# Performance work log

Measured on AMD Instinct MI355X. Metric: run time of the kernel, lower is better.

The kernel has to match this reference:

```python
import jax, jax.numpy as jnp
import numpy as np

TEMPERATURE = 0.04
LAMBDA_KOLEO = 0.1
EPS_NORM = 1e-12
EPS_KOLEO = 1e-9


def setup_inputs() -> dict:
    key = jax.random.key(0)
    k1, k2 = jax.random.split(key)
    N, D = 8192, 512
    z1 = jax.random.normal(k1, (N, D), dtype=jnp.float32)
    z2 = jax.random.normal(k2, (N, D), dtype=jnp.float32)
    return {"z1": z1, "z2": z2}


def _l2_normalize(x):
    # matches F.normalize(x, dim=1) with default eps=1e-12
    n = jnp.linalg.norm(x, axis=1, keepdims=True)
    return x / jnp.maximum(n, EPS_NORM)


def _infonce(queries, keys, temperature):
    # [N, N] similarity logits; labels are the diagonal
    logits = (queries @ keys.T) / temperature
    logp = jax.nn.log_softmax(logits, axis=1)
    return -jnp.mean(jnp.diagonal(logp))


def _koleo(emb):
    # pairwise euclidean distances via gram trick (matches torch.cdist p=2)
    sq = jnp.sum(emb * emb, axis=1)
    d2 = sq[:, None] + sq[None, :] - 2.0 * (emb @ emb.T)
    d = jnp.sqrt(jnp.maximum(d2, 0.0))
    N = emb.shape[0]
    eye = jnp.eye(N, dtype=bool)
    d = jnp.where(eye, jnp.inf, d)
    min_d = jnp.min(d, axis=1)
    return -jnp.mean(jnp.log(min_d + EPS_KOLEO))


def reference(z1, z2):
    z1 = _l2_normalize(z1)
    z2 = _l2_normalize(z2)
    loss_12 = _infonce(z1, z2, TEMPERATURE)
    loss_21 = _infonce(z2, z1, TEMPERATURE)
    loss_contrastive = (loss_12 + loss_21) / 2
    koleo_1 = _koleo(z1)
    koleo_2 = _koleo(z2)
    loss_koleo = (koleo_1 + koleo_2) / 2
    total_loss = loss_contrastive + LAMBDA_KOLEO * loss_koleo
    return total_loss
```

## Files before the change

### kernel.cpp

```cpp
#include <hip/hip_runtime.h>
#include <hip/hip_bf16.h>
#include <math.h>

#define N 8192
#define D 512
#define BM 128
#define BKB 128
#define NSTRIP 64
#define S_BLOCKS (NSTRIP * NSTRIP)
#define TRI (NSTRIP * (NSTRIP + 1) / 2)
#define G_BLOCKS (2 * TRI)
#define SG_BLOCKS (S_BLOCKS + G_BLOCKS)

typedef int i32x4 __attribute__((ext_vector_type(4)));

__device__ inline void gload_lds16(const void* g, void* l) {
  __builtin_amdgcn_global_load_lds(
      (const __attribute__((address_space(1))) void*)g,
      (__attribute__((address_space(3))) void*)l, 16, 0, 0);
}

__global__ __launch_bounds__(256) void norm_kernel(
    const float* __restrict__ z1, const float* __restrict__ z2,
    unsigned char* __restrict__ q1, unsigned char* __restrict__ q2,
    float* __restrict__ invs1, float* __restrict__ invs2,
    float* __restrict__ diag, float* __restrict__ out) {
  int row = blockIdx.x;
  int t = threadIdx.x;
  if (row == 0 && t == 0) out[0] = 0.0f;
  const float* a = z1 + (size_t)row * D;
  const float* b = z2 + (size_t)row * D;
  float va[2], vb[2];
  float ss1 = 0.f, ss2 = 0.f, dd = 0.f;
#pragma unroll
  for (int i = 0; i < 2; i++) {
    float x = a[t + 256 * i];
    float y = b[t + 256 * i];
    va[i] = x; vb[i] = y;
    ss1 += x * x; ss2 += y * y; dd += x * y;
  }
#pragma unroll
  for (int off = 1; off < 64; off <<= 1) {
    ss1 += __shfl_xor(ss1, off);
    ss2 += __shfl_xor(ss2, off);
    dd  += __shfl_xor(dd,  off);
  }
  __shared__ float red[3][4];
  int wv = t >> 6;
  if ((t & 63) == 0) { red[0][wv] = ss1; red[1][wv] = ss2; red[2][wv] = dd; }
  __syncthreads();
  ss1 = red[0][0] + red[0][1] + red[0][2] + red[0][3];
  ss2 = red[1][0] + red[1][1] + red[1][2] + red[1][3];
  dd  = red[2][0] + red[2][1] + red[2][2] + red[2][3];
  float i1 = 1.0f / fmaxf(sqrtf(ss1), 1e-12f);
  float i2 = 1.0f / fmaxf(sqrtf(ss2), 1e-12f);
  float m1 = 1e-30f, m2 = 1e-30f;
#pragma unroll
  for (int i = 0; i < 2; i++) {
    m1 = fmaxf(m1, fabsf(va[i] * i1));
    m2 = fmaxf(m2, fabsf(vb[i] * i2));
  }
#pragma unroll
  for (int off = 1; off < 64; off <<= 1) {
    m1 = fmaxf(m1, __shfl_xor(m1, off));
    m2 = fmaxf(m2, __shfl_xor(m2, off));
  }
  __syncthreads();
  if ((t & 63) == 0) { red[0][wv] = m1; red[1][wv] = m2; }
  __syncthreads();
  m1 = fmaxf(fmaxf(red[0][0], red[0][1]), fmaxf(red[0][2], red[0][3]));
  m2 = fmaxf(fmaxf(red[1][0], red[1][1]), fmaxf(red[1][2], red[1][3]));
  float s1 = 127.0f / m1, s2 = 127.0f / m2;
#pragma unroll
  for (int i = 0; i < 2; i++) {
    int qa = __float2int_rn(va[i] * i1 * s1);
    int qb = __float2int_rn(vb[i] * i2 * s2);
    q1[(size_t)row * D + t + 256 * i] = (unsigned char)qa;
    q2[(size_t)row * D + t + 256 * i] = (unsigned char)qb;
  }
  if (t == 0) {
    diag[row] = dd * i1 * i2;
    invs1[row] = m1 * (1.0f / 127.0f);
    invs2[row] = m2 * (1.0f / 127.0f);
  }
}

__device__ __forceinline__ void mm_tile_i8(
    const unsigned char* __restrict__ X, const unsigned char* __restrict__ Y,
    int r0, int c0, unsigned char* At, unsigned char* Bt, i32x4 (&acc)[4][4],
    int t, int lr, int quad, int rw, int cw) {
  const i32x4 izero = {0, 0, 0, 0};
#pragma unroll
  for (int i = 0; i < 4; i++)
#pragma unroll
    for (int j = 0; j < 4; j++) acc[i][j] = izero;

  for (int kc = 0; kc < 4; kc++) {
    int k0 = kc * BKB;
    __syncthreads();
#pragma unroll
    for (int it = 0; it < 4; it++) {
      int s = it * 256 + t;
      int row = s >> 3, cs = s & 7;
      int src = cs ^ (row & 7);
      gload_lds16(X + (size_t)(r0 + row) * D + k0 + src * 16, &At[s * 16]);
    }
#pragma unroll
    for (int it = 0; it < 4; it++) {
      int s = it * 256 + t;
      int row = s >> 3, cs = s & 7;
      int src = cs ^ (row & 7);
      gload_lds16(Y + (size_t)(c0 + row) * D + k0 + src * 16, &Bt[s * 16]);
    }
    __syncthreads();

#pragma unroll
    for (int step = 0; step < 2; step++) {
      i32x4 af[4], bf[4];
#pragma unroll
      for (int i = 0; i < 4; i++) {
        int row = rw * 64 + i * 16 + lr;
        int ps = (step * 4 + quad) ^ (row & 7);
        af[i] = *(const i32x4*)&At[row * BKB + ps * 16];
      }
#pragma unroll
      for (int j = 0; j < 4; j++) {
        int row = cw * 64 + j * 16 + lr;
        int ps = (step * 4 + quad) ^ (row & 7);
        bf[j] = *(const i32x4*)&Bt[row * BKB + ps * 16];
      }
#pragma unroll
      for (int i = 0; i < 4; i++)
#pragma unroll
        for (int j = 0; j < 4; j++)
          acc[i][j] = __builtin_amdgcn_mfma_i32_16x16x64_i8(af[i], bf[j], acc[i][j], 0, 0, 0);
    }
  }
}

__global__ __launch_bounds__(256, 3) void sg_kernel(
    const unsigned char* __restrict__ q1, const unsigned char* __restrict__ q2,
    const float* __restrict__ invs1, const float* __restrict__ invs2,
    float* __restrict__ rowS, float* __restrict__ colS,
    float* __restrict__ partG) {
  __shared__ unsigned char At[BM * BKB];
  __shared__ unsigned char Bt[BM * BKB];
  __shared__ float redA[2][BM];
  __shared__ float redB[2][BM];

  int bx = blockIdx.x;
  int t = threadIdx.x;
  int lane = t & 63;
  int wave = t >> 6;
  int quad = lane >> 4;
  int lr = lane & 15;
  int rw = wave >> 1;
  int cw = wave & 1;
  const float scalefac = 1.4426950408889634f / 0.04f;

  bool smode = bx < S_BLOCKS;
  const unsigned char* X;
  const unsigned char* Y;
  const float* ivA;
  const float* ivB;
  int r0, c0, ga = 0, gb = 0, gg = 0;
  bool diagb = false;
  if (smode) {
    r0 = (bx >> 6) * BM;
    c0 = (bx & 63) * BM;
    X = q1; Y = q2; ivA = invs1; ivB = invs2;
  } else {
    int gx = bx - S_BLOCKS;
    gg = (gx >= TRI) ? 1 : 0;
    int tri = gx - gg * TRI;
    int a = (int)((sqrtf(8.0f * (float)tri + 1.0f) - 1.0f) * 0.5f);
    while ((a + 1) * (a + 2) / 2 <= tri) a++;
    while (a * (a + 1) / 2 > tri) a--;
    int b = tri - a * (a + 1) / 2;
    ga = a; gb = b;
    X = gg ? q2 : q1; Y = X;
    ivA = gg ? invs2 : invs1; ivB = ivA;
    r0 = a * BM;
    c0 = b * BM;
    diagb = (a == b);
  }

  i32x4 acc[4][4];
  mm_tile_i8(X, Y, r0, c0, At, Bt, acc, t, lr, quad, rw, cw);

  float ia[4][4];
  float ib[4];
#pragma unroll
  for (int i = 0; i < 4; i++)
#pragma unroll
    for (int r = 0; r < 4; r++)
      ia[i][r] = ivA[r0 + rw * 64 + i * 16 + quad * 4 + r];
#pragma unroll
  for (int j = 0; j < 4; j++)
    ib[j] = ivB[c0 + cw * 64 + j * 16 + lr];

  if (smode) {
    float rowacc[4][4];
    float colacc[4] = {0.0f, 0.0f, 0.0f, 0.0f};
#pragma unroll
    for (int i = 0; i < 4; i++)
#pragma unroll
      for (int r = 0; r < 4; r++) rowacc[i][r] = 0.0f;
#pragma unroll
    for (int j = 0; j < 4; j++) ib[j] *= scalefac;
#pragma unroll
    for (int i = 0; i < 4; i++)
#pragma unroll
      for (int j = 0; j < 4; j++)
#pragma unroll
        for (int r = 0; r < 4; r++) {
          float e = __builtin_amdgcn_exp2f((float)acc[i][j][r] * ia[i][r] * ib[j]);
          rowacc[i][r] += e;
          colacc[j] += e;
        }
#pragma unroll
    for (int j = 0; j < 4; j++) {
      colacc[j] += __shfl_xor(colacc[j], 16);
      colacc[j] += __shfl_xor(colacc[j], 32);
    }
    if (lane < 16) {
#pragma unroll
      for (int j = 0; j < 4; j++) redA[rw][cw * 64 + j * 16 + lr] = colacc[j];
    }
    __syncthreads();
    if (t < BM) colS[(size_t)(r0 >> 7) * N + c0 + t] = redA[0][t] + redA[1][t];

#pragma unroll
    for (int i = 0; i < 4; i++)
#pragma unroll
      for (int r = 0; r < 4; r++) {
        float v = rowacc[i][r];
#pragma unroll
        for (int off = 1; off < 16; off <<= 1) v += __shfl_xor(v, off);
        if (lr == 0) redB[cw][rw * 64 + i * 16 + quad * 4 + r] = v;
      }
    __syncthreads();
    if (t < BM) rowS[(size_t)(c0 >> 7) * N + r0 + t] = redB[0][t] + redB[1][t];
  } else {
#pragma unroll
    for (int i = 0; i < 4; i++)
#pragma unroll
      for (int r = 0; r < 4; r++) {
        int rr = rw * 64 + i * 16 + quad * 4 + r;
        float v = -3.0e38f;
#pragma unroll
        for (int j = 0; j < 4; j++) {
          float x = (float)acc[i][j][r] * ib[j];
          int cc = cw * 64 + j * 16 + lr;
          if (diagb && cc == rr) x = -3.0e38f;
          v = fmaxf(v, x);
        }
#pragma unroll
        for (int off = 1; off < 16; off <<= 1) v = fmaxf(v, __shfl_xor(v, off));
        if (lr == 0) redA[cw][rr] = v * ia[i][r];
      }
    __syncthreads();
    if (t < BM)
      partG[((size_t)(gg * NSTRIP + gb)) * N + r0 + t] = fmaxf(redA[0][t], redA[1][t]);

    if (!diagb) {
#pragma unroll
      for (int j = 0; j < 4; j++) {
        float m = -3.0e38f;
#pragma unroll
        for (int i = 0; i < 4; i++)
#pragma unroll
          for (int r = 0; r < 4; r++) m = fmaxf(m, (float)acc[i][j][r] * ia[i][r]);
        m = fmaxf(m, __shfl_xor(m, 16));
        m = fmaxf(m, __shfl_xor(m, 32));
        if (lane < 16) redB[rw][cw * 64 + j * 16 + lr] = m * ib[j];
      }
      __syncthreads();
      if (t < BM)
        partG[((size_t)(gg * NSTRIP + ga)) * N + c0 + t] = fmaxf(redB[0][t], redB[1][t]);
    }
  }
}

__global__ __launch_bounds__(256) void combine_kernel(
    const float* __restrict__ diag,
    const float* __restrict__ rowS, const float* __restrict__ colS,
    const float* __restrict__ partG, float* __restrict__ out) {
  const float invT = 25.0f;
  int i = blockIdx.x * 256 + threadIdx.x;

  float s = 0.0f;
  for (int q = 0; q < NSTRIP; q++) s += rowS[(size_t)q * N + i];
  float a12 = logf(s) - diag[i] * invT;

  s = 0.0f;
  for (int o = 0; o < NSTRIP; o++) s += colS[(size_t)o * N + i];
  float a21 = logf(s) - diag[i] * invT;

  float g1 = -3.0e38f, g2 = -3.0e38f;
  for (int o = 0; o < NSTRIP; o++) {
    g1 = fmaxf(g1, partG[(size_t)o * N + i]);
    g2 = fmaxf(g2, partG[(size_t)(NSTRIP + o) * N + i]);
  }
  float k1 = logf(sqrtf(fmaxf(2.0f - 2.0f * g1, 0.0f)) + 1e-9f);
  float k2 = logf(sqrtf(fmaxf(2.0f - 2.0f * g2, 0.0f)) + 1e-9f);

  float c = 0.5f * (a12 + a21) / (float)N - 0.1f * 0.5f * (k1 + k2) / (float)N;
#pragma unroll
  for (int off = 1; off < 64; off <<= 1) c += __shfl_xor(c, off);
  __shared__ float fr[4];
  int wv = threadIdx.x >> 6;
  if ((threadIdx.x & 63) == 0) fr[wv] = c;
  __syncthreads();
  if (threadIdx.x == 0)
    atomicAdd(out, fr[0] + fr[1] + fr[2] + fr[3]);
}

extern "C" void kernel_launch(void* const* d_in, const int* in_sizes, int n_in,
                              void* d_out, int out_size, void* d_ws, size_t ws_size,
                              hipStream_t stream) {
  const float* z1 = (const float*)d_in[0];
  const float* z2 = (const float*)d_in[1];
  char* w = (char*)d_ws;
  unsigned char* q1 = (unsigned char*)w; w += (size_t)N * D;
  unsigned char* q2 = (unsigned char*)w; w += (size_t)N * D;
  float* invs1 = (float*)w;  w += (size_t)N * sizeof(float);
  float* invs2 = (float*)w;  w += (size_t)N * sizeof(float);
  float* diag = (float*)w;   w += (size_t)N * sizeof(float);
  float* rowS = (float*)w;   w += (size_t)NSTRIP * N * sizeof(float);
  float* colS = (float*)w;   w += (size_t)NSTRIP * N * sizeof(float);
  float* partG = (float*)w;  w += (size_t)2 * NSTRIP * N * sizeof(float);
  float* out = (float*)d_out;

  norm_kernel<<<N, 256, 0, stream>>>(z1, z2, q1, q2, invs1, invs2, diag, out);
  sg_kernel<<<SG_BLOCKS, 256, 0, stream>>>(q1, q2, invs1, invs2, rowS, colS, partG);
  combine_kernel<<<N / 256, 256, 0, stream>>>(diag, rowS, colS, partG, out);
}
```

Baseline: 202.2 us.

## Double-buffer int8 GEMM LDS tiles so global loads overlap MFMA compute

Splits the K loop into eight 64-byte chunks and alternates between two LDS buffer pairs. The loads for the next chunk are issued before the MFMAs on the current chunk, so global-to-LDS traffic can overlap compute instead of being followed by a full stall. The swizzle is adapted to 64-byte rows, and extra barriers are added before the epilogue reductions. Total LDS use stays the same. The gain depends on the barrier waiting for the async LDS loads correctly, and there are twice as many loop iterations, each with its own barrier.

```diff
diff --git a/kernel.cpp b/kernel.cpp
--- a/kernel.cpp
+++ b/kernel.cpp
@@ -5,7 +5,7 @@
 #define N 8192
 #define D 512
 #define BM 128
-#define BKB 128
+#define BK 64
 #define NSTRIP 64
 #define S_BLOCKS (NSTRIP * NSTRIP)
 #define TRI (NSTRIP * (NSTRIP + 1) / 2)
@@ -85,9 +85,22 @@
   }
 }
 
+__device__ __forceinline__ void stage_tile(
+    const unsigned char* __restrict__ P, int base, int k0,
+    unsigned char* T, int t) {
+#pragma unroll
+  for (int it = 0; it < 2; it++) {
+    int s = it * 256 + t;
+    int row = s >> 2, cs = s & 3;
+    int src = cs ^ ((row >> 1) & 3);
+    gload_lds16(P + (size_t)(base + row) * D + k0 + src * 16, &T[s * 16]);
+  }
+}
+
 __device__ __forceinline__ void mm_tile_i8(
     const unsigned char* __restrict__ X, const unsigned char* __restrict__ Y,
-    int r0, int c0, unsigned char* At, unsigned char* Bt, i32x4 (&acc)[4][4],
+    int r0, int c0, unsigned char* At0, unsigned char* Bt0,
+    unsigned char* At1, unsigned char* Bt1, i32x4 (&acc)[4][4],
     int t, int lr, int quad, int rw, int cw) {
   const i32x4 izero = {0, 0, 0, 0};
 #pragma unroll
@@ -95,46 +108,37 @@
 #pragma unroll
     for (int j = 0; j < 4; j++) acc[i][j] = izero;
 
-  for (int kc = 0; kc < 4; kc++) {
-    int k0 = kc * BKB;
-    __syncthreads();
-#pragma unroll
-    for (int it = 0; it < 4; it++) {
-      int s = it * 256 + t;
-      int row = s >> 3, cs = s & 7;
-      int src = cs ^ (row & 7);
-      gload_lds16(X + (size_t)(r0 + row) * D + k0 + src * 16, &At[s * 16]);
-    }
-#pragma unroll
-    for (int it = 0; it < 4; it++) {
-      int s = it * 256 + t;
-      int row = s >> 3, cs = s & 7;
-      int src = cs ^ (row & 7);
-      gload_lds16(Y + (size_t)(c0 + row) * D + k0 + src * 16, &Bt[s * 16]);
-    }
-    __syncthreads();
-
-#pragma unroll
-    for (int step = 0; step < 2; step++) {
-      i32x4 af[4], bf[4];
-#pragma unroll
-      for (int i = 0; i < 4; i++) {
-        int row = rw * 64 + i * 16 + lr;
-        int ps = (step * 4 + quad) ^ (row & 7);
-        af[i] = *(const i32x4*)&At[row * BKB + ps * 16];
-      }
-#pragma unroll
-      for (int j = 0; j < 4; j++) {
-        int row = cw * 64 + j * 16 + lr;
-        int ps = (step * 4 + quad) ^ (row & 7);
-        bf[j] = *(const i32x4*)&Bt[row * BKB + ps * 16];
-      }
-#pragma unroll
-      for (int i = 0; i < 4; i++)
-#pragma unroll
-        for (int j = 0; j < 4; j++)
-          acc[i][j] = __builtin_amdgcn_mfma_i32_16x16x64_i8(af[i], bf[j], acc[i][j], 0, 0, 0);
-    }
+  stage_tile(X, r0, 0, At0, t);
+  stage_tile(Y, c0, 0, Bt0, t);
+
+  for (int kc = 0; kc < 8; kc++) {
+    unsigned char* Ac = (kc & 1) ? At1 : At0;
+    unsigned char* Bc = (kc & 1) ? Bt1 : Bt0;
+    unsigned char* An = (kc & 1) ? At0 : At1;
+    unsigned char* Bn = (kc & 1) ? Bt0 : Bt1;
+    __syncthreads();
+    if (kc < 7) {
+      stage_tile(X, r0, (kc + 1) * BK, An, t);
+      stage_tile(Y, c0, (kc + 1) * BK, Bn, t);
+    }
+    i32x4 af[4], bf[4];
+#pragma unroll
+    for (int i = 0; i < 4; i++) {
+      int row = rw * 64 + i * 16 + lr;
+      int ps = quad ^ ((row >> 1) & 3);
+      af[i] = *(const i32x4*)&Ac[row * 64 + ps * 16];
+    }
+#pragma unroll
+    for (int j = 0; j < 4; j++) {
+      int row = cw * 64 + j * 16 + lr;
+      int ps = quad ^ ((row >> 1) & 3);
+      bf[j] = *(const i32x4*)&Bc[row * 64 + ps * 16];
+    }
+#pragma unroll
+    for (int i = 0; i < 4; i++)
+#pragma unroll
+      for (int j = 0; j < 4; j++)
+        acc[i][j] = __builtin_amdgcn_mfma_i32_16x16x64_i8(af[i], bf[j], acc[i][j], 0, 0, 0);
   }
 }
 
@@ -143,8 +147,10 @@
     const float* __restrict__ invs1, const float* __restrict__ invs2,
     float* __restrict__ rowS, float* __restrict__ colS,
     float* __restrict__ partG) {
-  __shared__ unsigned char At[BM * BKB];
-  __shared__ unsigned char Bt[BM * BKB];
+  __shared__ unsigned char At0[BM * BK];
+  __shared__ unsigned char Bt0[BM * BK];
+  __shared__ unsigned char At1[BM * BK];
+  __shared__ unsigned char Bt1[BM * BK];
   __shared__ float redA[2][BM];
   __shared__ float redB[2][BM];
 
@@ -186,7 +192,7 @@
   }
 
   i32x4 acc[4][4];
-  mm_tile_i8(X, Y, r0, c0, At, Bt, acc, t, lr, quad, rw, cw);
+  mm_tile_i8(X, Y, r0, c0, At0, Bt0, At1, Bt1, acc, t, lr, quad, rw, cw);
 
   float ia[4][4];
   float ib[4];
@@ -223,6 +229,7 @@
       colacc[j] += __shfl_xor(colacc[j], 16);
       colacc[j] += __shfl_xor(colacc[j], 32);
     }
+    __syncthreads();
     if (lane < 16) {
 #pragma unroll
       for (int j = 0; j < 4; j++) redA[rw][cw * 64 + j * 16 + lr] = colacc[j];
@@ -242,6 +249,7 @@
     __syncthreads();
     if (t < BM) rowS[(size_t)(c0 >> 7) * N + r0 + t] = redB[0][t] + redB[1][t];
   } else {
+    __syncthreads();
 #pragma unroll
     for (int i = 0; i < 4; i++)
 #pragma unroll
```

After: 204.8 us. Within noise of the previous version (+1.2%).
